# Kernel optimization log

Measured on AMD Instinct MI355X. Metric: run time of the kernel, lower is better.

The kernel has to match this reference:

```python
import jax, jax.numpy as jnp
import numpy as np

B, Hp, Wp, DIM, NH = 2, 64, 64, 128, 4
N = Hp * Wp

def _rel_index(H, W):
    ch, cw = np.meshgrid(np.arange(H), np.arange(W), indexing='ij')
    coords = np.stack([ch.ravel(), cw.ravel()])            # [2, N]
    rel = coords[:, :, None] - coords[:, None, :]          # [2, N, N]
    rel = rel.transpose(1, 2, 0)
    rel[:, :, 0] += H - 1
    rel[:, :, 1] += W - 1
    rel[:, :, 0] *= 2 * W - 1
    return jnp.asarray(rel.sum(-1), dtype=jnp.int32)       # [N, N]

def setup_inputs() -> dict:
    key = jax.random.key(0)
    ks = jax.random.split(key, 8)
    d = {}
    d['x'] = jax.random.normal(ks[0], (B, N, DIM), dtype=jnp.float32)
    d['q_w'] = jax.random.normal(ks[1], (DIM, DIM), dtype=jnp.float32) * 0.02
    d['q_b'] = jnp.zeros((DIM,), dtype=jnp.float32)
    d['kv_w'] = jax.random.normal(ks[2], (2 * DIM, DIM), dtype=jnp.float32) * 0.02
    d['kv_b'] = jnp.zeros((2 * DIM,), dtype=jnp.float32)
    d['proj_w'] = jax.random.normal(ks[3], (DIM, DIM), dtype=jnp.float32) * 0.02
    d['proj_b'] = jnp.zeros((DIM,), dtype=jnp.float32)
    d['bias_table'] = jax.random.normal(ks[4], ((2 * Hp - 1) * (2 * Wp - 1), NH), dtype=jnp.float32) * 0.02
    d['rel_index'] = _rel_index(Hp, Wp)
    d['H'] = Hp
    d['W'] = Wp
    return d

def reference(x, q_w, q_b, kv_w, kv_b, proj_w, proj_b, bias_table, rel_index, H, W):
    Bz, Nn, C = x.shape
    h = bias_table.shape[1]
    dh = C // h
    scale = dh ** -0.5
    # torch Linear: y = x @ W^T + b
    q = (x @ q_w.T + q_b).reshape(Bz, Nn, h, dh).transpose(0, 2, 1, 3)          # [B,h,N,d]
    kv = (x @ kv_w.T + kv_b).reshape(Bz, Nn, 2, h, dh).transpose(2, 0, 3, 1, 4) # [2,B,h,N,d]
    k, v = kv[0], kv[1]
    attn = jnp.einsum('bhnd,bhmd->bhnm', q, k) * scale                           # [B,h,N,N]
    bias = bias_table[rel_index]                                                 # [N,N,h] gather
    attn = attn + jnp.transpose(bias, (2, 0, 1))[None]
    attn = jax.nn.softmax(attn, axis=-1)
    out = jnp.einsum('bhnm,bhmd->bhnd', attn, v)
    out = out.transpose(0, 2, 1, 3).reshape(Bz, Nn, C)
    out = out @ proj_w.T + proj_b
    return out, attn
```

## Files before the change

### kernel.cpp

```cpp
#include <hip/hip_runtime.h>
#include <hip/hip_bf16.h>


typedef short s16x8 __attribute__((ext_vector_type(8)));
typedef float f32x4 __attribute__((ext_vector_type(4)));

#define LOG2E 1.4426950408889634f
#define SCALE_L2 (0.17677669529663687f * LOG2E)

__device__ __forceinline__ float bf2f(short u) {
  union { unsigned int i; float f; } v;
  v.i = ((unsigned int)(unsigned short)u) << 16;
  return v.f;
}
__device__ __forceinline__ short f2bf(float f) {
  union { float f; unsigned int i; } v; v.f = f;
  unsigned int r = v.i + 0x7FFFu + ((v.i >> 16) & 1u);
  return (short)(r >> 16);
}

__global__ __launch_bounds__(256)
void bt_kernel(const float* __restrict__ bias_table, short* __restrict__ bt16) {
  int idx = blockIdx.x * 256 + threadIdx.x;
  int h = blockIdx.y;
  if (idx < 16129) bt16[h * 16129 + idx] = f2bf(bias_table[idx * 4 + h] * LOG2E);
}

__global__ __launch_bounds__(256)
void qkv_kernel(const float* __restrict__ x,
                const float* __restrict__ q_w, const float* __restrict__ q_b,
                const float* __restrict__ kv_w, const float* __restrict__ kv_b,
                short* __restrict__ q16, short* __restrict__ kTile, short* __restrict__ vTile)
{
  __shared__ float xs[16][128];
  const int tid = threadIdx.x;
  const int row0 = blockIdx.x * 16;
  {
    const float4* src = (const float4*)(x + (size_t)row0 * 128);
    float4* dst = (float4*)&xs[0][0];
    dst[tid]       = src[tid];
    dst[tid + 256] = src[tid + 256];
  }
  __syncthreads();

  const int b  = row0 >> 12;
  const int nn0 = row0 & 4095;
  const int ctb = nn0 >> 4;

  {
    const int oc = tid;
    const float* wrow = (oc < 128) ? (q_w + (size_t)oc*128) : (kv_w + (size_t)(oc-128)*128);
    const float bias = (oc < 128) ? q_b[oc] : kv_b[oc-128];
    float acc[16];
    #pragma unroll
    for (int r = 0; r < 16; ++r) acc[r] = bias;
    const float4* w4 = (const float4*)wrow;
    #pragma unroll 4
    for (int k4 = 0; k4 < 32; ++k4) {
      float4 wv = w4[k4];
      #pragma unroll
      for (int r = 0; r < 16; ++r) {
        float4 xv = *(const float4*)&xs[r][k4 << 2];
        acc[r] = fmaf(xv.x, wv.x, acc[r]); acc[r] = fmaf(xv.y, wv.y, acc[r]);
        acc[r] = fmaf(xv.z, wv.z, acc[r]); acc[r] = fmaf(xv.w, wv.w, acc[r]);
      }
    }
    if (oc < 128) {
      const int hh = oc >> 5, d = oc & 31;
      short* dstp = q16 + ((size_t)((b<<2) + hh)*4096 + nn0)*32 + d;
      #pragma unroll
      for (int r = 0; r < 16; ++r) dstp[(size_t)r * 32] = f2bf(acc[r]);
    } else {
      const int j = oc - 128, hh = j >> 5, d32 = j & 31;
      const int lg = d32 >> 3, e = d32 & 7;
      short* dstp = kTile + ((((size_t)((b<<2)+hh)*256 + ctb)*64) + (lg<<4))*8 + e;
      #pragma unroll
      for (int r = 0; r < 16; ++r) dstp[(size_t)r * 8] = f2bf(acc[r]);
    }
  }

  {
    const int vd = tid & 127;
    const int rb = (tid >> 7) << 3;
    const float* wrow = kv_w + (size_t)(128 + vd)*128;
    float acc[8];
    const float bias = kv_b[128 + vd];
    #pragma unroll
    for (int r = 0; r < 8; ++r) acc[r] = bias;
    const float4* w4 = (const float4*)wrow;
    #pragma unroll 4
    for (int k4 = 0; k4 < 32; ++k4) {
      float4 wv = w4[k4];
      #pragma unroll
      for (int r = 0; r < 8; ++r) {
        float4 xv = *(const float4*)&xs[rb + r][k4 << 2];
        acc[r] = fmaf(xv.x, wv.x, acc[r]); acc[r] = fmaf(xv.y, wv.y, acc[r]);
        acc[r] = fmaf(xv.z, wv.z, acc[r]); acc[r] = fmaf(xv.w, wv.w, acc[r]);
      }
    }
    const int hh = vd >> 5, dv = vd & 31;
    const int half = dv >> 4, l15v = dv & 15;
    short* base = vTile + (((size_t)((b<<2)+hh)*256 + ctb)*64)*8;
    #pragma unroll
    for (int r = 0; r < 8; ++r) {
      int m15 = rb + r;
      int lg = m15 >> 2, e = (m15 & 3) + (half << 2);
      base[(size_t)((lg<<4) + l15v)*8 + e] = f2bf(acc[r]);
    }
  }
}

__global__ __launch_bounds__(256, 8)
void attn_pv_kernel(const short* __restrict__ q16, const short* __restrict__ kTile,
                    const short* __restrict__ vTile, const short* __restrict__ bt16,
                    float* __restrict__ outp, float* __restrict__ inv_ws)
{
  __shared__ float accL[4][64][9];
  __shared__ float wsum[4][16];
  __shared__ float invL[16];

  const int tid  = threadIdx.x;
  const int wv   = tid >> 6;
  const int lane = tid & 63;
  const int l15  = lane & 15;
  const int lg   = lane >> 4;
  const int bh   = blockIdx.x & 7;
  const int row0 = (blockIdx.x >> 3) << 4;
  const int h    = bh & 3;
  const int b    = bh >> 2;

  const short* kt  = kTile + (size_t)bh * (256*512);
  const short* vt  = vTile + (size_t)bh * (256*512);
  const short* bth = bt16 + h * 16129;

  s16x8 qfrag = *(const s16x8*)(q16 + (size_t)bh*(4096*32) + (size_t)(row0 + l15)*32 + (lg<<3));
  const int rn = row0 >> 6;
  const int c0 = row0 & 63;
  const int lanoff = l15 - (lg << 2);

  f32x4 acc0a = {0.f,0.f,0.f,0.f}, acc0b = {0.f,0.f,0.f,0.f};
  f32x4 acc1a = {0.f,0.f,0.f,0.f}, acc1b = {0.f,0.f,0.f,0.f};
  float sum = 0.f;

  #define PASS_A_BODY(CT, A0, A1)                                              \
  {                                                                            \
    s16x8 kfrag = *(const s16x8*)(kt + (size_t)(CT)*512 + (lane<<3));          \
    f32x4 z = {0.f,0.f,0.f,0.f};                                               \
    f32x4 d = __builtin_amdgcn_mfma_f32_16x16x32_bf16(kfrag, qfrag, z, 0,0,0); \
    int sidx = (rn - ((CT)>>2) + 63)*127 + (c0 - (((CT)&3)<<4) + 63);          \
    const short* bp = bth + (sidx + lanoff);                                   \
    float e0 = __builtin_amdgcn_exp2f(fmaf(d[0], SCALE_L2, bf2f(bp[ 0])));     \
    float e1 = __builtin_amdgcn_exp2f(fmaf(d[1], SCALE_L2, bf2f(bp[-1])));     \
    float e2 = __builtin_amdgcn_exp2f(fmaf(d[2], SCALE_L2, bf2f(bp[-2])));     \
    float e3 = __builtin_amdgcn_exp2f(fmaf(d[3], SCALE_L2, bf2f(bp[-3])));     \
    sum += (e0+e1) + (e2+e3);                                                  \
    s16x8 pfrag;                                                               \
    pfrag[0]=f2bf(e0); pfrag[1]=f2bf(e1); pfrag[2]=f2bf(e2); pfrag[3]=f2bf(e3);\
    pfrag[4]=0; pfrag[5]=0; pfrag[6]=0; pfrag[7]=0;                            \
    s16x8 vv = *(const s16x8*)(vt + (size_t)(CT)*512 + (lane<<3));             \
    s16x8 vfa = {vv[0],vv[1],vv[2],vv[3],0,0,0,0};                             \
    s16x8 vfb = {vv[4],vv[5],vv[6],vv[7],0,0,0,0};                             \
    A0 = __builtin_amdgcn_mfma_f32_16x16x32_bf16(pfrag, vfa, A0, 0, 0, 0);     \
    A1 = __builtin_amdgcn_mfma_f32_16x16x32_bf16(pfrag, vfb, A1, 0, 0, 0);     \
  }

  const int ct0 = wv << 6;
  #pragma unroll 2
  for (int i2 = 0; i2 < 32; ++i2) {
    PASS_A_BODY(ct0 + 2*i2,     acc0a, acc1a)
    PASS_A_BODY(ct0 + 2*i2 + 1, acc0b, acc1b)
  }
  #undef PASS_A_BODY

  f32x4 acc0 = acc0a + acc0b;
  f32x4 acc1 = acc1a + acc1b;

  sum += __shfl_xor(sum, 16);
  sum += __shfl_xor(sum, 32);
  if (lg == 0) wsum[wv][l15] = sum;
  #pragma unroll
  for (int j = 0; j < 4; ++j) {
    accL[wv][lane][j]     = acc0[j];
    accL[wv][lane][4 + j] = acc1[j];
  }
  __syncthreads();

  if (tid < 16) {
    float t = (wsum[0][tid] + wsum[1][tid]) + (wsum[2][tid] + wsum[3][tid]);
    float iv = 1.0f / t;
    invL[tid] = iv;
    inv_ws[(size_t)bh*4096 + row0 + tid] = iv;
  }
  __syncthreads();

  if (wv == 0) {
    float* os = outp + ((size_t)(b*4096 + row0))*128 + (h<<5);
    #pragma unroll
    for (int s = 0; s < 8; ++s) {
      int j = s & 3, half = s >> 2;
      float v = (accL[0][lane][s] + accL[1][lane][s])
              + (accL[2][lane][s] + accL[3][lane][s]);
      int r = (lg << 2) + j;
      os[(size_t)r*128 + (half << 4) + l15] = v * invL[r];
    }
  }
}

__global__ __launch_bounds__(256, 8)
void attn_wr_kernel(const short* __restrict__ q16, const short* __restrict__ kTile,
                    const short* __restrict__ bt16, const float* __restrict__ inv_ws,
                    float* __restrict__ attn)
{
  __shared__ float stage[4][16][64];

  const int tid  = threadIdx.x;
  const int wv   = tid >> 6;
  const int lane = tid & 63;
  const int l15  = lane & 15;
  const int lg   = lane >> 4;
  const int bh   = blockIdx.x & 7;
  const int row0 = (blockIdx.x >> 3) << 4;
  const int h    = bh & 3;

  const short* kt  = kTile + (size_t)bh * (256*512);
  const short* bth = bt16 + h * 16129;

  s16x8 qfrag = *(const s16x8*)(q16 + (size_t)bh*(4096*32) + (size_t)(row0 + l15)*32 + (lg<<3));
  const int rn = row0 >> 6;
  const int c0 = row0 & 63;
  const int lanoff = l15 - (lg << 2);
  const float inv = inv_ws[(size_t)bh*4096 + row0 + l15];

  float (*st)[64] = stage[wv];
  const int ct0 = wv << 6;

  const int srow = lane >> 4;
  const int c4r  = lane & 15;

  for (int g = 0; g < 16; ++g) {
    #pragma unroll
    for (int t = 0; t < 4; ++t) {
      const int ct = ct0 + (g << 2) + t;
      s16x8 kfrag = *(const s16x8*)(kt + (size_t)ct*512 + (lane<<3));
      f32x4 z = {0.f,0.f,0.f,0.f};
      f32x4 d = __builtin_amdgcn_mfma_f32_16x16x32_bf16(kfrag, qfrag, z, 0, 0, 0);
      int sidx = (rn - (ct>>2) + 63)*127 + (c0 - ((ct&3)<<4) + 63);
      const short* bp = bth + (sidx + lanoff);
      float o0 = __builtin_amdgcn_exp2f(fmaf(d[0], SCALE_L2, bf2f(bp[ 0]))) * inv;
      float o1 = __builtin_amdgcn_exp2f(fmaf(d[1], SCALE_L2, bf2f(bp[-1]))) * inv;
      float o2 = __builtin_amdgcn_exp2f(fmaf(d[2], SCALE_L2, bf2f(bp[-2]))) * inv;
      float o3 = __builtin_amdgcn_exp2f(fmaf(d[3], SCALE_L2, bf2f(bp[-3]))) * inv;
      const int c4 = (t << 2) + lg;
      float* p = &st[l15][(c4 ^ l15) << 2];
      p[0] = o0; p[1] = o1; p[2] = o2; p[3] = o3;
    }
    const size_t gcol = (size_t)(ct0 + (g << 2)) << 4;
    #pragma unroll
    for (int rg = 0; rg < 4; ++rg) {
      const int rr = (rg << 2) + srow;
      f32x4 o = *(const f32x4*)&st[rr][(c4r ^ rr) << 2];
      float* dst = attn + ((size_t)(bh*4096 + row0 + rr))*4096 + gcol + (c4r << 2);
      __builtin_nontemporal_store(o, (f32x4*)dst);
    }
  }
}

__global__ __launch_bounds__(256)
void proj_kernel(float* __restrict__ out, const float* __restrict__ proj_w,
                 const float* __restrict__ proj_b)
{
  __shared__ float xs[16][128];
  const int tid = threadIdx.x;
  const int row0 = blockIdx.x * 16;
  {
    const float4* src = (const float4*)(out + (size_t)row0 * 128);
    float4* dst = (float4*)&xs[0][0];
    dst[tid]       = src[tid];
    dst[tid + 256] = src[tid + 256];
  }
  __syncthreads();
  const int oc = tid & 127;
  const int rb = (tid >> 7) << 3;
  float acc[8];
  const float bias = proj_b[oc];
  #pragma unroll
  for (int r = 0; r < 8; ++r) acc[r] = bias;
  const float4* w4 = (const float4*)(proj_w + (size_t)oc*128);
  #pragma unroll 4
  for (int k4 = 0; k4 < 32; ++k4) {
    float4 wv = w4[k4];
    #pragma unroll
    for (int r = 0; r < 8; ++r) {
      float4 xv = *(const float4*)&xs[rb + r][k4 << 2];
      acc[r] = fmaf(xv.x, wv.x, acc[r]); acc[r] = fmaf(xv.y, wv.y, acc[r]);
      acc[r] = fmaf(xv.z, wv.z, acc[r]); acc[r] = fmaf(xv.w, wv.w, acc[r]);
    }
  }
  #pragma unroll
  for (int r = 0; r < 8; ++r)
    out[(size_t)(row0 + rb + r)*128 + oc] = acc[r];
}

extern "C" void kernel_launch(void* const* d_in, const int* in_sizes, int n_in,
                              void* d_out, int out_size, void* d_ws, size_t ws_size,
                              hipStream_t stream) {
  const float* x          = (const float*)d_in[0];
  const float* q_w        = (const float*)d_in[1];
  const float* q_b        = (const float*)d_in[2];
  const float* kv_w       = (const float*)d_in[3];
  const float* kv_b       = (const float*)d_in[4];
  const float* proj_w     = (const float*)d_in[5];
  const float* proj_b     = (const float*)d_in[6];
  const float* bias_table = (const float*)d_in[7];

  float* out  = (float*)d_out;
  float* attn = (float*)d_out + 1048576;

  char* ws = (char*)d_ws;
  short* q16    = (short*)(ws);
  short* kTile  = (short*)(ws + (2u << 20));
  short* vTile  = (short*)(ws + (4u << 20));
  short* bt16   = (short*)(ws + 6291456);
  float* inv_ws = (float*)(ws + 6420992);

  bt_kernel<<<dim3(64, 4), dim3(256), 0, stream>>>(bias_table, bt16);
  qkv_kernel<<<dim3(512), dim3(256), 0, stream>>>(x, q_w, q_b, kv_w, kv_b, q16, kTile, vTile);
  attn_pv_kernel<<<dim3(2048), dim3(256), 0, stream>>>(q16, kTile, vTile, bt16, out, inv_ws);
  attn_wr_kernel<<<dim3(2048), dim3(256), 0, stream>>>(q16, kTile, bt16, inv_ws, attn);
  proj_kernel<<<dim3(512), dim3(256), 0, stream>>>(out, proj_w, proj_b);
}
```

Baseline: 222.5 us.

## Use fp32 bias table, packed bf16 converts, K16 MFMA, MFMA row-sums, split QKV grid

The bias table is now stored in fp32, so each lane fetches its four bias values with one unaligned vector load instead of four scalar bf16 loads. The P·V products use 16x16x16 MFMAs with a packed hardware bf16 convert, which removes the zero-padded K=32 operands and the manual rounding code. Softmax row sums are computed by an extra MFMA against a vector of ones instead of scalar adds and shuffles. The QKV kernel is split over two grid slices, one computing Q/K and the other V, to double parallelism. Trade-offs: the bias table takes twice the workspace, unaligned loads may split across cache lines, and the row sums now add bf16-rounded probabilities, which changes numerics slightly.

```diff
diff --git a/kernel.cpp b/kernel.cpp
--- a/kernel.cpp
+++ b/kernel.cpp
@@ -3,27 +3,40 @@
 
 
 typedef short s16x8 __attribute__((ext_vector_type(8)));
+typedef short s16x4 __attribute__((ext_vector_type(4)));
 typedef float f32x4 __attribute__((ext_vector_type(4)));
+typedef float f32x4u __attribute__((ext_vector_type(4), aligned(4)));
+typedef unsigned u32x2 __attribute__((ext_vector_type(2)));
 
 #define LOG2E 1.4426950408889634f
 #define SCALE_L2 (0.17677669529663687f * LOG2E)
 
-__device__ __forceinline__ float bf2f(short u) {
-  union { unsigned int i; float f; } v;
-  v.i = ((unsigned int)(unsigned short)u) << 16;
-  return v.f;
-}
 __device__ __forceinline__ short f2bf(float f) {
   union { float f; unsigned int i; } v; v.f = f;
   unsigned int r = v.i + 0x7FFFu + ((v.i >> 16) & 1u);
   return (short)(r >> 16);
 }
+__device__ __forceinline__ unsigned cvt_pk_bf16(float lo, float hi) {
+  unsigned r;
+  asm("v_cvt_pk_bf16_f32 %0, %1, %2" : "=v"(r) : "v"(lo), "v"(hi));
+  return r;
+}
+
+__device__ __forceinline__ f32x4 pv_mfma(s16x4 a, s16x4 b, f32x4 c) {
+#if __has_builtin(__builtin_amdgcn_mfma_f32_16x16x16bf16_1k)
+  return __builtin_amdgcn_mfma_f32_16x16x16bf16_1k(a, b, c, 0, 0, 0);
+#else
+  s16x8 a8 = {a[0], a[1], a[2], a[3], 0, 0, 0, 0};
+  s16x8 b8 = {b[0], b[1], b[2], b[3], 0, 0, 0, 0};
+  return __builtin_amdgcn_mfma_f32_16x16x32_bf16(a8, b8, c, 0, 0, 0);
+#endif
+}
 
 __global__ __launch_bounds__(256)
-void bt_kernel(const float* __restrict__ bias_table, short* __restrict__ bt16) {
+void bt_kernel(const float* __restrict__ bias_table, float* __restrict__ bt) {
   int idx = blockIdx.x * 256 + threadIdx.x;
   int h = blockIdx.y;
-  if (idx < 16129) bt16[h * 16129 + idx] = f2bf(bias_table[idx * 4 + h] * LOG2E);
+  if (idx < 16129) bt[h * 16129 + idx] = bias_table[idx * 4 + h] * LOG2E;
 }
 
 __global__ __launch_bounds__(256)
@@ -47,7 +60,7 @@
   const int nn0 = row0 & 4095;
   const int ctb = nn0 >> 4;
 
-  {
+  if (blockIdx.y == 0) {
     const int oc = tid;
     const float* wrow = (oc < 128) ? (q_w + (size_t)oc*128) : (kv_w + (size_t)(oc-128)*128);
     const float bias = (oc < 128) ? q_b[oc] : kv_b[oc-128];
@@ -77,9 +90,7 @@
       #pragma unroll
       for (int r = 0; r < 16; ++r) dstp[(size_t)r * 8] = f2bf(acc[r]);
     }
-  }
-
-  {
+  } else {
     const int vd = tid & 127;
     const int rb = (tid >> 7) << 3;
     const float* wrow = kv_w + (size_t)(128 + vd)*128;
@@ -112,7 +123,7 @@
 
 __global__ __launch_bounds__(256, 8)
 void attn_pv_kernel(const short* __restrict__ q16, const short* __restrict__ kTile,
-                    const short* __restrict__ vTile, const short* __restrict__ bt16,
+                    const short* __restrict__ vTile, const float* __restrict__ bt,
                     float* __restrict__ outp, float* __restrict__ inv_ws)
 {
   __shared__ float accL[4][64][9];
@@ -131,16 +142,18 @@
 
   const short* kt  = kTile + (size_t)bh * (256*512);
   const short* vt  = vTile + (size_t)bh * (256*512);
-  const short* bth = bt16 + h * 16129;
+  const float* bth = bt + h * 16129;
 
   s16x8 qfrag = *(const s16x8*)(q16 + (size_t)bh*(4096*32) + (size_t)(row0 + l15)*32 + (lg<<3));
   const int rn = row0 >> 6;
   const int c0 = row0 & 63;
   const int lanoff = l15 - (lg << 2);
 
+  const s16x4 ones4 = {(short)0x3F80, (short)0x3F80, (short)0x3F80, (short)0x3F80};
+
   f32x4 acc0a = {0.f,0.f,0.f,0.f}, acc0b = {0.f,0.f,0.f,0.f};
   f32x4 acc1a = {0.f,0.f,0.f,0.f}, acc1b = {0.f,0.f,0.f,0.f};
-  float sum = 0.f;
+  f32x4 acc_s = {0.f,0.f,0.f,0.f};
 
   #define PASS_A_BODY(CT, A0, A1)                                              \
   {                                                                            \
@@ -148,20 +161,19 @@
     f32x4 z = {0.f,0.f,0.f,0.f};                                               \
     f32x4 d = __builtin_amdgcn_mfma_f32_16x16x32_bf16(kfrag, qfrag, z, 0,0,0); \
     int sidx = (rn - ((CT)>>2) + 63)*127 + (c0 - (((CT)&3)<<4) + 63);          \
-    const short* bp = bth + (sidx + lanoff);                                   \
-    float e0 = __builtin_amdgcn_exp2f(fmaf(d[0], SCALE_L2, bf2f(bp[ 0])));     \
-    float e1 = __builtin_amdgcn_exp2f(fmaf(d[1], SCALE_L2, bf2f(bp[-1])));     \
-    float e2 = __builtin_amdgcn_exp2f(fmaf(d[2], SCALE_L2, bf2f(bp[-2])));     \
-    float e3 = __builtin_amdgcn_exp2f(fmaf(d[3], SCALE_L2, bf2f(bp[-3])));     \
-    sum += (e0+e1) + (e2+e3);                                                  \
-    s16x8 pfrag;                                                               \
-    pfrag[0]=f2bf(e0); pfrag[1]=f2bf(e1); pfrag[2]=f2bf(e2); pfrag[3]=f2bf(e3);\
-    pfrag[4]=0; pfrag[5]=0; pfrag[6]=0; pfrag[7]=0;                            \
+    f32x4u w = *(const f32x4u*)(bth + sidx + lanoff - 3);                      \
+    float e0 = __builtin_amdgcn_exp2f(fmaf(d[0], SCALE_L2, w[3]));             \
+    float e1 = __builtin_amdgcn_exp2f(fmaf(d[1], SCALE_L2, w[2]));             \
+    float e2 = __builtin_amdgcn_exp2f(fmaf(d[2], SCALE_L2, w[1]));             \
+    float e3 = __builtin_amdgcn_exp2f(fmaf(d[3], SCALE_L2, w[0]));             \
+    u32x2 pk = {cvt_pk_bf16(e0, e1), cvt_pk_bf16(e2, e3)};                     \
+    s16x4 pfrag = __builtin_bit_cast(s16x4, pk);                               \
     s16x8 vv = *(const s16x8*)(vt + (size_t)(CT)*512 + (lane<<3));             \
-    s16x8 vfa = {vv[0],vv[1],vv[2],vv[3],0,0,0,0};                             \
-    s16x8 vfb = {vv[4],vv[5],vv[6],vv[7],0,0,0,0};                             \
-    A0 = __builtin_amdgcn_mfma_f32_16x16x32_bf16(pfrag, vfa, A0, 0, 0, 0);     \
-    A1 = __builtin_amdgcn_mfma_f32_16x16x32_bf16(pfrag, vfb, A1, 0, 0, 0);     \
+    s16x4 vfa = __builtin_shufflevector(vv, vv, 0, 1, 2, 3);                   \
+    s16x4 vfb = __builtin_shufflevector(vv, vv, 4, 5, 6, 7);                   \
+    A0 = pv_mfma(pfrag, vfa, A0);                                              \
+    A1 = pv_mfma(pfrag, vfb, A1);                                              \
+    acc_s = pv_mfma(pfrag, ones4, acc_s);                                      \
   }
 
   const int ct0 = wv << 6;
@@ -175,9 +187,10 @@
   f32x4 acc0 = acc0a + acc0b;
   f32x4 acc1 = acc1a + acc1b;
 
-  sum += __shfl_xor(sum, 16);
-  sum += __shfl_xor(sum, 32);
-  if (lg == 0) wsum[wv][l15] = sum;
+  if (l15 == 0) {
+    #pragma unroll
+    for (int j = 0; j < 4; ++j) wsum[wv][(lg << 2) + j] = acc_s[j];
+  }
   #pragma unroll
   for (int j = 0; j < 4; ++j) {
     accL[wv][lane][j]     = acc0[j];
@@ -208,7 +221,7 @@
 
 __global__ __launch_bounds__(256, 8)
 void attn_wr_kernel(const short* __restrict__ q16, const short* __restrict__ kTile,
-                    const short* __restrict__ bt16, const float* __restrict__ inv_ws,
+                    const float* __restrict__ bt, const float* __restrict__ inv_ws,
                     float* __restrict__ attn)
 {
   __shared__ float stage[4][16][64];
@@ -223,7 +236,7 @@
   const int h    = bh & 3;
 
   const short* kt  = kTile + (size_t)bh * (256*512);
-  const short* bth = bt16 + h * 16129;
+  const float* bth = bt + h * 16129;
 
   s16x8 qfrag = *(const s16x8*)(q16 + (size_t)bh*(4096*32) + (size_t)(row0 + l15)*32 + (lg<<3));
   const int rn = row0 >> 6;
@@ -245,11 +258,11 @@
       f32x4 z = {0.f,0.f,0.f,0.f};
       f32x4 d = __builtin_amdgcn_mfma_f32_16x16x32_bf16(kfrag, qfrag, z, 0, 0, 0);
       int sidx = (rn - (ct>>2) + 63)*127 + (c0 - ((ct&3)<<4) + 63);
-      const short* bp = bth + (sidx + lanoff);
-      float o0 = __builtin_amdgcn_exp2f(fmaf(d[0], SCALE_L2, bf2f(bp[ 0]))) * inv;
-      float o1 = __builtin_amdgcn_exp2f(fmaf(d[1], SCALE_L2, bf2f(bp[-1]))) * inv;
-      float o2 = __builtin_amdgcn_exp2f(fmaf(d[2], SCALE_L2, bf2f(bp[-2]))) * inv;
-      float o3 = __builtin_amdgcn_exp2f(fmaf(d[3], SCALE_L2, bf2f(bp[-3]))) * inv;
+      f32x4u w = *(const f32x4u*)(bth + sidx + lanoff - 3);
+      float o0 = __builtin_amdgcn_exp2f(fmaf(d[0], SCALE_L2, w[3])) * inv;
+      float o1 = __builtin_amdgcn_exp2f(fmaf(d[1], SCALE_L2, w[2])) * inv;
+      float o2 = __builtin_amdgcn_exp2f(fmaf(d[2], SCALE_L2, w[1])) * inv;
+      float o3 = __builtin_amdgcn_exp2f(fmaf(d[3], SCALE_L2, w[0])) * inv;
       const int c4 = (t << 2) + lg;
       float* p = &st[l15][(c4 ^ l15) << 2];
       p[0] = o0; p[1] = o1; p[2] = o2; p[3] = o3;
@@ -320,12 +333,12 @@
   short* q16    = (short*)(ws);
   short* kTile  = (short*)(ws + (2u << 20));
   short* vTile  = (short*)(ws + (4u << 20));
-  short* bt16   = (short*)(ws + 6291456);
-  float* inv_ws = (float*)(ws + 6420992);
-
-  bt_kernel<<<dim3(64, 4), dim3(256), 0, stream>>>(bias_table, bt16);
-  qkv_kernel<<<dim3(512), dim3(256), 0, stream>>>(x, q_w, q_b, kv_w, kv_b, q16, kTile, vTile);
-  attn_pv_kernel<<<dim3(2048), dim3(256), 0, stream>>>(q16, kTile, vTile, bt16, out, inv_ws);
-  attn_wr_kernel<<<dim3(2048), dim3(256), 0, stream>>>(q16, kTile, bt16, inv_ws, attn);
+  float* bt     = (float*)(ws + 6291456);
+  float* inv_ws = (float*)(ws + 6549520);
+
+  bt_kernel<<<dim3(64, 4), dim3(256), 0, stream>>>(bias_table, bt);
+  qkv_kernel<<<dim3(512, 2), dim3(256), 0, stream>>>(x, q_w, q_b, kv_w, kv_b, q16, kTile, vTile);
+  attn_pv_kernel<<<dim3(2048), dim3(256), 0, stream>>>(q16, kTile, vTile, bt, out, inv_ws);
+  attn_wr_kernel<<<dim3(2048), dim3(256), 0, stream>>>(q16, kTile, bt, inv_ws, attn);
   proj_kernel<<<dim3(512), dim3(256), 0, stream>>>(out, proj_w, proj_b);
 }
```

After: 205.6 us. 7.6% less time.
